# Performance work log

Hardware: AMD Instinct MI355X
Metric: run time of the kernel (lower is better)

Reference implementation:

```python
import jax, jax.numpy as jnp
import numpy as np

EPS = 1e-6
CLIP_RATIO = 1.0  # input_clip_ratio


def fwht(x):
    """Fast Walsh-Hadamard transform along last dim (N must be a power of 2).
    Unnormalized; caller divides by sqrt(N) (QuaRot OnlineHadamard convention)."""
    m, n = x.shape
    h = 1
    y = x
    while h < n:  # log2(n) fixed iterations, fine under jit
        y = y.reshape(m, n // (2 * h), 2, h)
        a, b = y[:, :, 0, :], y[:, :, 1, :]
        y = jnp.concatenate([a + b, a - b], axis=-1)  # [m, n//(2h), 2h]
        h *= 2
    return y.reshape(m, n)


def setup_inputs() -> dict:
    key = jax.random.key(0)
    k1, k2, k3 = jax.random.split(key, 3)
    M, IN, OUT = 8192, 4096, 4096
    x = jax.random.normal(k1, (M, IN), dtype=jnp.float32)
    weight = jax.random.normal(k2, (OUT, IN), dtype=jnp.float32) * 0.02
    bias = jax.random.normal(k3, (OUT,), dtype=jnp.float32) * 0.01
    return {"x": x, "weight": weight, "bias": bias}


def reference(x, weight, bias):
    # --- offline weight quantization (quantize_from_float) ---
    # per-output-row symmetric int4: scale = max|w| / 7, clamp min 1e-6
    w_scales = jnp.clip(jnp.max(jnp.abs(weight), axis=1, keepdims=True), EPS, None) / 7.0  # [OUT,1]
    qw = jnp.clip(jnp.round(weight / w_scales), -8, 7)  # int4 values kept in fp32 (exact)

    # --- online Hadamard rotation of activations ---
    n = x.shape[-1]
    x2 = fwht(x) * (1.0 / jnp.sqrt(jnp.float32(n)))

    # --- symmetric per-token int4 activation quantization (QuaRot Quantizer) ---
    sx = jnp.clip(jnp.max(jnp.abs(x2), axis=-1, keepdims=True), EPS, None) * (CLIP_RATIO / 7.0)  # [M,1]
    qx = jnp.clip(jnp.round(x2 / sx), -8, 7)

    qy = jnp.einsum('mk,nk->mn', qx, qw)  # [M, OUT]

    # --- sym_dequant: row scale (activation) * column scale (weight) + bias ---
    y = qy * sx * w_scales.T + bias[None, :]
    return y
```

## Files before the change

### kernel.cpp

```cpp
#include <hip/hip_runtime.h>
#include <cstdint>

#define QEPS 1e-6f

typedef int v4i __attribute__((ext_vector_type(4)));
typedef int v8i __attribute__((ext_vector_type(8)));
typedef float v4f __attribute__((ext_vector_type(4)));

__device__ __forceinline__ void gl_lds16(const void* g, void* l) {
  __builtin_amdgcn_global_load_lds(
      (const __attribute__((address_space(1))) void*)g,
      (__attribute__((address_space(3))) void*)l, 16, 0, 0);
}

__device__ __forceinline__ uint8_t enc_e4m3(float q) {
  const int idx = (int)q + 8;
  const unsigned long long lo = 0xB8C0C4C8CACCCED0ull;
  const unsigned long long hi = 0x4E4C4A4844403800ull;
  const unsigned long long tbl = (idx < 8) ? lo : hi;
  return (uint8_t)(tbl >> ((idx & 7) * 8));
}

__global__ __launch_bounds__(256) void wquant_kernel(const float* __restrict__ w,
                                                     uint8_t* __restrict__ qw,
                                                     float* __restrict__ wscale) {
  const int n = blockIdx.x;
  const int t = threadIdx.x;
  const float4* wrow = (const float4*)(w + (size_t)n * 4096);
  float4 v[4];
  float am = 0.f;
#pragma unroll
  for (int i = 0; i < 4; ++i) {
    v[i] = wrow[i * 256 + t];
    am = fmaxf(am, fmaxf(fmaxf(fabsf(v[i].x), fabsf(v[i].y)),
                         fmaxf(fabsf(v[i].z), fabsf(v[i].w))));
  }
#pragma unroll
  for (int off = 32; off > 0; off >>= 1)
    am = fmaxf(am, __shfl_down(am, off));
  __shared__ float wm[4];
  if ((t & 63) == 0) wm[t >> 6] = am;
  __syncthreads();
  const float rowmax = fmaxf(fmaxf(wm[0], wm[1]), fmaxf(wm[2], wm[3]));
  const float scale = fmaxf(rowmax, QEPS) / 7.0f;
  if (t == 0) wscale[n] = scale;
  uchar4* qrow = (uchar4*)(qw + (size_t)n * 4096);
#pragma unroll
  for (int i = 0; i < 4; ++i) {
    uchar4 q;
    q.x = enc_e4m3(fminf(fmaxf(rintf(v[i].x / scale), -8.f), 7.f));
    q.y = enc_e4m3(fminf(fmaxf(rintf(v[i].y / scale), -8.f), 7.f));
    q.z = enc_e4m3(fminf(fmaxf(rintf(v[i].z / scale), -8.f), 7.f));
    q.w = enc_e4m3(fminf(fmaxf(rintf(v[i].w / scale), -8.f), 7.f));
    qrow[i * 256 + t] = q;
  }
}

__global__ __launch_bounds__(256) void xquant_kernel(const float* __restrict__ x,
                                                     uint8_t* __restrict__ qx,
                                                     float* __restrict__ sx) {
  const int m = blockIdx.x * 4 + (threadIdx.x >> 6);
  const int g = threadIdx.x & 63;
  const float4* xrow = (const float4*)(x + (size_t)m * 4096);
  float4 v[16];
#pragma unroll
  for (int j = 0; j < 16; ++j) v[j] = xrow[j * 64 + g];

#pragma unroll
  for (int j = 0; j < 16; ++j) {
    float a0 = v[j].x, b0 = v[j].y, a1 = v[j].z, b1 = v[j].w;
    v[j].x = a0 + b0; v[j].y = a0 - b0;
    v[j].z = a1 + b1; v[j].w = a1 - b1;
  }
#pragma unroll
  for (int j = 0; j < 16; ++j) {
    float a0 = v[j].x, b0 = v[j].z, a1 = v[j].y, b1 = v[j].w;
    v[j].x = a0 + b0; v[j].z = a0 - b0;
    v[j].y = a1 + b1; v[j].w = a1 - b1;
  }
#pragma unroll
  for (int d = 1; d < 64; d <<= 1) {
    const bool low = (g & d) == 0;
#pragma unroll
    for (int j = 0; j < 16; ++j) {
      float px = __shfl_xor(v[j].x, d);
      float py = __shfl_xor(v[j].y, d);
      float pz = __shfl_xor(v[j].z, d);
      float pw = __shfl_xor(v[j].w, d);
      v[j].x = low ? (v[j].x + px) : (px - v[j].x);
      v[j].y = low ? (v[j].y + py) : (py - v[j].y);
      v[j].z = low ? (v[j].z + pz) : (pz - v[j].z);
      v[j].w = low ? (v[j].w + pw) : (pw - v[j].w);
    }
  }
#pragma unroll
  for (int d = 1; d < 16; d <<= 1) {
#pragma unroll
    for (int j = 0; j < 16; ++j) {
      if ((j & d) == 0) {
        float4 a = v[j], b = v[j + d];
        v[j].x = a.x + b.x; v[j].y = a.y + b.y;
        v[j].z = a.z + b.z; v[j].w = a.w + b.w;
        v[j + d].x = a.x - b.x; v[j + d].y = a.y - b.y;
        v[j + d].z = a.z - b.z; v[j + d].w = a.w - b.w;
      }
    }
  }

  float am = 0.f;
#pragma unroll
  for (int j = 0; j < 16; ++j)
    am = fmaxf(am, fmaxf(fmaxf(fabsf(v[j].x), fabsf(v[j].y)),
                         fmaxf(fabsf(v[j].z), fabsf(v[j].w))));
#pragma unroll
  for (int off = 32; off > 0; off >>= 1)
    am = fmaxf(am, __shfl_xor(am, off));

  const float inv64 = 1.0f / 64.0f;
  const float sxv = fmaxf(am * inv64, QEPS) * (1.0f / 7.0f);
  if (g == 0) sx[m] = sxv;

  uchar4* qrow = (uchar4*)(qx + (size_t)m * 4096);
#pragma unroll
  for (int j = 0; j < 16; ++j) {
    uchar4 q;
    q.x = enc_e4m3(fminf(fmaxf(rintf((v[j].x * inv64) / sxv), -8.f), 7.f));
    q.y = enc_e4m3(fminf(fmaxf(rintf((v[j].y * inv64) / sxv), -8.f), 7.f));
    q.z = enc_e4m3(fminf(fmaxf(rintf((v[j].z * inv64) / sxv), -8.f), 7.f));
    q.w = enc_e4m3(fminf(fmaxf(rintf((v[j].w * inv64) / sxv), -8.f), 7.f));
    qrow[j * 64 + g] = q;
  }
}

#define BM 256
#define BN 256
#define BK 128

union frag_u { v8i v; v4i h[2]; };

#define MFMA_Q(MB, NB)                                                        \
  do {                                                                        \
    __builtin_amdgcn_s_setprio(1);                                            \
    _Pragma("unroll") for (int i_ = 0; i_ < 4; ++i_)                          \
        _Pragma("unroll") for (int j_ = 0; j_ < 2; ++j_)                      \
            acc[(MB) + i_][(NB) + j_] =                                       \
                __builtin_amdgcn_mfma_scale_f32_16x16x128_f8f6f4(             \
                    a[i_].v, b[j_].v, acc[(MB) + i_][(NB) + j_], 0, 0, 0,     \
                    0x7F7F7F7F, 0, 0x7F7F7F7F);                               \
    __builtin_amdgcn_s_setprio(0);                                            \
  } while (0)

#define LDA4(BASE)                                                            \
  do {                                                                        \
    _Pragma("unroll") for (int i_ = 0; i_ < 4; ++i_) {                        \
      const int o_ = arow[(BASE) + i_];                                       \
      a[i_].h[0] = *(const v4i*)(As_c + o_);                                  \
      a[i_].h[1] = *(const v4i*)(As_c + (o_ ^ 16));                           \
    }                                                                         \
  } while (0)

#define LDB2(BASE)                                                            \
  do {                                                                        \
    _Pragma("unroll") for (int j_ = 0; j_ < 2; ++j_) {                        \
      const int o_ = brow[(BASE) + j_];                                       \
      b[j_].h[0] = *(const v4i*)(Bs_c + o_);                                  \
      b[j_].h[1] = *(const v4i*)(Bs_c + (o_ ^ 16));                           \
    }                                                                         \
  } while (0)

__global__ __launch_bounds__(512, 2) void gemm_kernel(const uint8_t* __restrict__ qx,
                                                      const uint8_t* __restrict__ qw,
                                                      const float* __restrict__ sx,
                                                      const float* __restrict__ wscale,
                                                      const float* __restrict__ bias,
                                                      float* __restrict__ out) {
  __shared__ uint8_t As[2][BM * BK] __attribute__((aligned(16)));
  __shared__ uint8_t Bs[2][BN * BK] __attribute__((aligned(16)));

  const int t = threadIdx.x;
  const int bid = blockIdx.y * gridDim.x + blockIdx.x;
  const int swz = ((bid & 7) << 6) | (bid >> 3);
  const int bx = swz & 15;
  const int by = swz >> 4;
  const int m0 = by * BM;
  const int n0 = bx * BN;

  const int lane = t & 63;
  const int wave = t >> 6;
  const int wr = wave >> 2;
  const int wc = wave & 3;
  const int lr = lane & 15;
  const int lq = lane >> 4;
  const int r7 = lr & 7;
  const int c0 = ((2 * lq) ^ r7) << 4;

  v4f acc[8][4] = {};

  const int rA = t >> 3;
  const int csrc = (((t & 7) ^ (rA & 7)) << 4);
  const uint8_t* ga = qx + (size_t)(m0 + rA) * 4096 + csrc;
  const uint8_t* gb = qw + (size_t)(n0 + rA) * 4096 + csrc;
  const int ldst = t * 16;

  int arow[8], brow[4];
#pragma unroll
  for (int mt = 0; mt < 8; ++mt)
    arow[mt] = (wr * 128 + mt * 16 + lr) * BK + c0;
#pragma unroll
  for (int nt = 0; nt < 4; ++nt)
    brow[nt] = (wc * 64 + nt * 16 + lr) * BK + c0;

#pragma unroll
  for (int s = 0; s < 4; ++s) {
    gl_lds16(ga + (size_t)s * 64 * 4096, As[0] + s * 8192 + ldst);
    gl_lds16(gb + (size_t)s * 64 * 4096, Bs[0] + s * 8192 + ldst);
  }
  __syncthreads();

  for (int kt = 0; kt < 32; ++kt) {
    const uint8_t* As_c = As[kt & 1];
    const uint8_t* Bs_c = Bs[kt & 1];
    frag_u a[4], b[2];

    LDA4(0);
    LDB2(0);
    if (kt < 31) {
      const int koff = (kt + 1) << 7;
      uint8_t* Ad = As[(kt & 1) ^ 1];
      uint8_t* Bd = Bs[(kt & 1) ^ 1];
#pragma unroll
      for (int s = 0; s < 4; ++s) {
        gl_lds16(ga + (size_t)s * 64 * 4096 + koff, Ad + s * 8192 + ldst);
        gl_lds16(gb + (size_t)s * 64 * 4096 + koff, Bd + s * 8192 + ldst);
      }
    }
    __builtin_amdgcn_s_barrier();
    asm volatile("s_waitcnt lgkmcnt(0)" ::: "memory");
    MFMA_Q(0, 0);
    __builtin_amdgcn_s_barrier();

    LDB2(2);
    __builtin_amdgcn_s_barrier();
    asm volatile("s_waitcnt lgkmcnt(0)" ::: "memory");
    MFMA_Q(0, 2);
    __builtin_amdgcn_s_barrier();

    LDA4(4);
    __builtin_amdgcn_s_barrier();
    asm volatile("s_waitcnt lgkmcnt(0)" ::: "memory");
    MFMA_Q(4, 2);
    __builtin_amdgcn_s_barrier();

    LDB2(0);
    __builtin_amdgcn_s_barrier();
    asm volatile("s_waitcnt lgkmcnt(0)" ::: "memory");
    MFMA_Q(4, 0);
    __syncthreads();
  }

  float wv[4], bv[4];
#pragma unroll
  for (int nt = 0; nt < 4; ++nt) {
    const int n = n0 + wc * 64 + nt * 16 + lr;
    wv[nt] = wscale[n];
    bv[nt] = bias[n];
  }
#pragma unroll
  for (int mt = 0; mt < 8; ++mt) {
#pragma unroll
    for (int r = 0; r < 4; ++r) {
      const int m = m0 + wr * 128 + mt * 16 + lq * 4 + r;
      const float sm = sx[m];
#pragma unroll
      for (int nt = 0; nt < 4; ++nt) {
        const int n = n0 + wc * 64 + nt * 16 + lr;
        out[(size_t)m * 4096 + n] = acc[mt][nt][r] * sm * wv[nt] + bv[nt];
      }
    }
  }
}

extern "C" void kernel_launch(void* const* d_in, const int* in_sizes, int n_in,
                              void* d_out, int out_size, void* d_ws, size_t ws_size,
                              hipStream_t stream) {
  const float* x = (const float*)d_in[0];
  const float* w = (const float*)d_in[1];
  const float* bias = (const float*)d_in[2];
  float* out = (float*)d_out;

  uint8_t* qx = (uint8_t*)d_ws;
  uint8_t* qw = qx + (size_t)8192 * 4096;
  float* wscale = (float*)(qw + (size_t)4096 * 4096);
  float* sxp = wscale + 4096;

  wquant_kernel<<<4096, 256, 0, stream>>>(w, qw, wscale);
  xquant_kernel<<<2048, 256, 0, stream>>>(x, qx, sxp);
  dim3 grid(4096 / BN, 8192 / BM);
  gemm_kernel<<<grid, 512, 0, stream>>>(qx, qw, sxp, wscale, bias, out);
}
```

Baseline: 424.1 us.

## Prefetch two K-tiles ahead with explicit vmcnt waits in int4 GEMM

Restructures the GEMM main loop so global-to-LDS loads for tile kt+2 are issued into the buffer just consumed, after its last LDS reads, instead of loading tile kt+1 at the start of each iteration. Two tiles are staged up front, and each iteration ends with s_waitcnt vmcnt(8) plus a barrier rather than a full __syncthreads, so one tile's loads stay in flight across iterations. The intent is to hide more global memory latency behind MFMA work. It relies on manual waitcnt and sched_barrier placement being correct for buffer reuse safety.

```diff
diff --git a/kernel.cpp b/kernel.cpp
--- a/kernel.cpp
+++ b/kernel.cpp
@@ -168,6 +168,14 @@
     }                                                                         \
   } while (0)
 
+#define STAGE8(ABUF, BBUF, KOFF)                                              \
+  do {                                                                        \
+    _Pragma("unroll") for (int s_ = 0; s_ < 4; ++s_) {                        \
+      gl_lds16(ga + (size_t)s_ * 64 * 4096 + (KOFF), (ABUF) + s_ * 8192 + ldst); \
+      gl_lds16(gb + (size_t)s_ * 64 * 4096 + (KOFF), (BBUF) + s_ * 8192 + ldst); \
+    }                                                                         \
+  } while (0)
+
 __global__ __launch_bounds__(512, 2) void gemm_kernel(const uint8_t* __restrict__ qx,
                                                       const uint8_t* __restrict__ qw,
                                                       const float* __restrict__ sx,
@@ -210,12 +218,14 @@
   for (int nt = 0; nt < 4; ++nt)
     brow[nt] = (wc * 64 + nt * 16 + lr) * BK + c0;
 
-#pragma unroll
-  for (int s = 0; s < 4; ++s) {
-    gl_lds16(ga + (size_t)s * 64 * 4096, As[0] + s * 8192 + ldst);
-    gl_lds16(gb + (size_t)s * 64 * 4096, Bs[0] + s * 8192 + ldst);
-  }
-  __syncthreads();
+  STAGE8(As[0], Bs[0], 0);
+  __builtin_amdgcn_sched_barrier(0);
+  STAGE8(As[1], Bs[1], 128);
+  __builtin_amdgcn_sched_barrier(0);
+  asm volatile("s_waitcnt vmcnt(8)" ::: "memory");
+  __builtin_amdgcn_sched_barrier(0);
+  __builtin_amdgcn_s_barrier();
+  __builtin_amdgcn_sched_barrier(0);
 
   for (int kt = 0; kt < 32; ++kt) {
     const uint8_t* As_c = As[kt & 1];
@@ -224,16 +234,6 @@
 
     LDA4(0);
     LDB2(0);
-    if (kt < 31) {
-      const int koff = (kt + 1) << 7;
-      uint8_t* Ad = As[(kt & 1) ^ 1];
-      uint8_t* Bd = Bs[(kt & 1) ^ 1];
-#pragma unroll
-      for (int s = 0; s < 4; ++s) {
-        gl_lds16(ga + (size_t)s * 64 * 4096 + koff, Ad + s * 8192 + ldst);
-        gl_lds16(gb + (size_t)s * 64 * 4096 + koff, Bd + s * 8192 + ldst);
-      }
-    }
     __builtin_amdgcn_s_barrier();
     asm volatile("s_waitcnt lgkmcnt(0)" ::: "memory");
     MFMA_Q(0, 0);
@@ -253,9 +253,21 @@
 
     LDB2(0);
     __builtin_amdgcn_s_barrier();
+    __builtin_amdgcn_sched_barrier(0);
+    if (kt < 30) {
+      STAGE8(As[kt & 1], Bs[kt & 1], (kt + 2) << 7);
+    }
     asm volatile("s_waitcnt lgkmcnt(0)" ::: "memory");
     MFMA_Q(4, 0);
-    __syncthreads();
+    __builtin_amdgcn_sched_barrier(0);
+    if (kt < 30) {
+      asm volatile("s_waitcnt vmcnt(8)" ::: "memory");
+    } else {
+      asm volatile("s_waitcnt vmcnt(0)" ::: "memory");
+    }
+    __builtin_amdgcn_sched_barrier(0);
+    __builtin_amdgcn_s_barrier();
+    __builtin_amdgcn_sched_barrier(0);
   }
 
   float wv[4], bv[4];
```

Measured after the change: 448.5 us. +5.8%, slower.

## Restructure GEMM K-loop into two MFMA halves with later global prefetch

Applied to the files above, without the earlier changes.

The inner K-loop of the fp8/int4 GEMM goes from four quarter phases (4x2 MFMAs each, with B fragments reloaded) to two half phases (4x4 MFMAs each), loading all four B fragments once per K tile. The global-to-LDS prefetch of the next tile moves from the start of the iteration to the second phase. This cuts barriers and redundant LDS reads of B per tile. In exchange it holds more fragment registers live, which may pressure occupancy at 2 blocks per CU, and the prefetch issues later, so it has less time to hide latency.

```diff
diff --git a/kernel.cpp b/kernel.cpp
--- a/kernel.cpp
+++ b/kernel.cpp
@@ -138,14 +138,14 @@
 
 union frag_u { v8i v; v4i h[2]; };
 
-#define MFMA_Q(MB, NB)                                                        \
+#define MFMA_HALF(MB)                                                         \
   do {                                                                        \
     __builtin_amdgcn_s_setprio(1);                                            \
     _Pragma("unroll") for (int i_ = 0; i_ < 4; ++i_)                          \
-        _Pragma("unroll") for (int j_ = 0; j_ < 2; ++j_)                      \
-            acc[(MB) + i_][(NB) + j_] =                                       \
+        _Pragma("unroll") for (int j_ = 0; j_ < 4; ++j_)                      \
+            acc[(MB) + i_][j_] =                                              \
                 __builtin_amdgcn_mfma_scale_f32_16x16x128_f8f6f4(             \
-                    a[i_].v, b[j_].v, acc[(MB) + i_][(NB) + j_], 0, 0, 0,     \
+                    a[i_].v, b[j_].v, acc[(MB) + i_][j_], 0, 0, 0,            \
                     0x7F7F7F7F, 0, 0x7F7F7F7F);                               \
     __builtin_amdgcn_s_setprio(0);                                            \
   } while (0)
@@ -159,12 +159,20 @@
     }                                                                         \
   } while (0)
 
-#define LDB2(BASE)                                                            \
-  do {                                                                        \
-    _Pragma("unroll") for (int j_ = 0; j_ < 2; ++j_) {                        \
-      const int o_ = brow[(BASE) + j_];                                       \
+#define LDB4                                                                  \
+  do {                                                                        \
+    _Pragma("unroll") for (int j_ = 0; j_ < 4; ++j_) {                        \
+      const int o_ = brow[j_];                                                \
       b[j_].h[0] = *(const v4i*)(Bs_c + o_);                                  \
       b[j_].h[1] = *(const v4i*)(Bs_c + (o_ ^ 16));                           \
+    }                                                                         \
+  } while (0)
+
+#define STAGE8(ABUF, BBUF, KOFF)                                              \
+  do {                                                                        \
+    _Pragma("unroll") for (int s_ = 0; s_ < 4; ++s_) {                        \
+      gl_lds16(ga + (size_t)s_ * 64 * 4096 + (KOFF), (ABUF) + s_ * 8192 + ldst); \
+      gl_lds16(gb + (size_t)s_ * 64 * 4096 + (KOFF), (BBUF) + s_ * 8192 + ldst); \
     }                                                                         \
   } while (0)
 
@@ -210,51 +218,28 @@
   for (int nt = 0; nt < 4; ++nt)
     brow[nt] = (wc * 64 + nt * 16 + lr) * BK + c0;
 
-#pragma unroll
-  for (int s = 0; s < 4; ++s) {
-    gl_lds16(ga + (size_t)s * 64 * 4096, As[0] + s * 8192 + ldst);
-    gl_lds16(gb + (size_t)s * 64 * 4096, Bs[0] + s * 8192 + ldst);
-  }
+  STAGE8(As[0], Bs[0], 0);
   __syncthreads();
 
   for (int kt = 0; kt < 32; ++kt) {
     const uint8_t* As_c = As[kt & 1];
     const uint8_t* Bs_c = Bs[kt & 1];
-    frag_u a[4], b[2];
+    frag_u a[4], b[4];
 
     LDA4(0);
-    LDB2(0);
-    if (kt < 31) {
-      const int koff = (kt + 1) << 7;
-      uint8_t* Ad = As[(kt & 1) ^ 1];
-      uint8_t* Bd = Bs[(kt & 1) ^ 1];
-#pragma unroll
-      for (int s = 0; s < 4; ++s) {
-        gl_lds16(ga + (size_t)s * 64 * 4096 + koff, Ad + s * 8192 + ldst);
-        gl_lds16(gb + (size_t)s * 64 * 4096 + koff, Bd + s * 8192 + ldst);
-      }
-    }
+    LDB4;
     __builtin_amdgcn_s_barrier();
     asm volatile("s_waitcnt lgkmcnt(0)" ::: "memory");
-    MFMA_Q(0, 0);
+    MFMA_HALF(0);
     __builtin_amdgcn_s_barrier();
 
-    LDB2(2);
+    LDA4(4);
+    if (kt < 31) {
+      STAGE8(As[(kt & 1) ^ 1], Bs[(kt & 1) ^ 1], (kt + 1) << 7);
+    }
     __builtin_amdgcn_s_barrier();
     asm volatile("s_waitcnt lgkmcnt(0)" ::: "memory");
-    MFMA_Q(0, 2);
-    __builtin_amdgcn_s_barrier();
-
-    LDA4(4);
-    __builtin_amdgcn_s_barrier();
-    asm volatile("s_waitcnt lgkmcnt(0)" ::: "memory");
-    MFMA_Q(4, 2);
-    __builtin_amdgcn_s_barrier();
-
-    LDB2(0);
-    __builtin_amdgcn_s_barrier();
-    asm volatile("s_waitcnt lgkmcnt(0)" ::: "memory");
-    MFMA_Q(4, 0);
+    MFMA_HALF(4);
     __syncthreads();
   }
 
```

Result: faster. 414.9 us (-2.2%).
